# Kernel optimization log

Hardware: AMD Instinct MI355X
Metric: run time of the kernel (lower is better)

## Reference

```python
import jax, jax.numpy as jnp
import numpy as np

B, N, D, G = 32, 1024, 512, 32  # batch, set size, in_features, num_gaussians


def setup_inputs() -> dict:
    key = jax.random.key(0)
    k1, k2 = jax.random.split(key)
    minibatch = jax.random.normal(k1, (B, N, D), dtype=jnp.float32)
    # xavier_uniform for Linear(D -> G)
    limit = float(np.sqrt(6.0 / (D + G)))
    W_pi = jax.random.uniform(k2, (G, D), dtype=jnp.float32, minval=-limit, maxval=limit)
    b_pi = jnp.zeros((G,), dtype=jnp.float32)
    return {"minibatch": minibatch, "W_pi": W_pi, "b_pi": b_pi}


def reference(minibatch, W_pi, b_pi):
    d = minibatch.shape[-1]
    o = d // 2
    # mixture weights per (batch, sample): softmax over gaussian axis
    logits = jnp.einsum('bnd,gd->bng', minibatch, W_pi) + b_pi  # [B,N,G]
    pi = jax.nn.softmax(logits, axis=2)
    mu = minibatch[:, :, :o]        # [B,N,O]
    sigma = minibatch[:, :, -o:]    # [B,N,O]
    weights = jnp.mean(pi, axis=1)  # [B,G]
    denom = jnp.sum(pi, axis=1)     # [B,G]
    # weighted first moment -> locs (vectorized over all gaussians at once)
    m1 = jnp.einsum('bng,bno->bgo', pi, mu)                 # [B,G,O]
    locs = m1 / denom[:, :, None]                            # [B,G,O]
    # weighted E[mu^2 + sigma^2]; variance = E[mu^2+sigma^2] - locs^2
    # (identical math to sum(pi*((locs-mu)^2 + sigma^2))/sum(pi))
    m2 = jnp.einsum('bng,bno->bgo', pi, mu * mu + sigma * sigma)
    var = m2 / denom[:, :, None] - locs * locs
    scales = jnp.sqrt(jnp.maximum(var, 0.0))                 # [B,G,O]
    return weights, scales, locs
```

## Files before the change

kernel.cpp:

```cpp
#include <hip/hip_runtime.h>
#include <stdint.h>

#define B_ 32
#define N_ 1024
#define D_ 512
#define G_ 32

typedef __attribute__((ext_vector_type(8))) short short8;
typedef __attribute__((ext_vector_type(4))) float f32x4;
union U4S8 { uint4 u; short8 s; };

#define WS_M   524288
#define WS_DN  2621440

__device__ inline uint32_t pack_bf16x2(float a, float b) {
  uint32_t ua = __float_as_uint(a);
  uint32_t ub = __float_as_uint(b);
  ua += 0x7FFFu + ((ua >> 16) & 1u);
  ub += 0x7FFFu + ((ub >> 16) & 1u);
  return (ua >> 16) | (ub & 0xFFFF0000u);
}
__device__ inline uint16_t bf16r(float a) {
  uint32_t u = __float_as_uint(a);
  u += 0x7FFFu + ((u >> 16) & 1u);
  return (uint16_t)(u >> 16);
}

__global__ __launch_bounds__(256, 2) void mdn_k1(
    const float* __restrict__ x, const float* __restrict__ W,
    const float* __restrict__ bpi, float* ws)
{
  __shared__ uint32_t Wb[8192];
  __shared__ uint32_t SPT[1024];
  __shared__ float wpart[4][32];

  const int t = threadIdx.x;
  const int bid = blockIdx.x;
  const int b = bid >> 4;
  const int n0 = (bid & 15) * 64;
  const int w = t >> 6;
  const int lane = t & 63;

  #pragma unroll
  for (int i = 0; i < 8; ++i) {
    int s = t + i * 256;
    int g = s >> 6;
    int d0 = (s & 63) * 8;
    const float4* src = (const float4*)(W + g * D_ + d0);
    float4 f0 = src[0], f1 = src[1];
    int ks = d0 >> 5, ksub = (d0 >> 3) & 3;
    uint4 v;
    v.x = pack_bf16x2(f0.x, f0.y); v.y = pack_bf16x2(f0.z, f0.w);
    v.z = pack_bf16x2(f1.x, f1.y); v.w = pack_bf16x2(f1.z, f1.w);
    *(uint4*)(Wb + (size_t)(((ks * 4 + ksub) * 32 + g) * 4)) = v;
  }
  __syncthreads();

  const float* abase =
      x + ((size_t)(b * N_ + n0 + w * 16 + (lane & 15))) * D_ + (lane >> 4) * 8;

  f32x4 acc0 = {0.f, 0.f, 0.f, 0.f};
  f32x4 acc1 = {0.f, 0.f, 0.f, 0.f};

  float4 fa[16], fb[16];
  #pragma unroll
  for (int ks = 0; ks < 16; ++ks) {
    fa[ks] = *(const float4*)(abase + ks * 32);
    fb[ks] = *(const float4*)(abase + ks * 32 + 4);
  }
  #pragma unroll
  for (int ks = 0; ks < 16; ++ks) {
    U4S8 a;
    a.u.x = pack_bf16x2(fa[ks].x, fa[ks].y);
    a.u.y = pack_bf16x2(fa[ks].z, fa[ks].w);
    a.u.z = pack_bf16x2(fb[ks].x, fb[ks].y);
    a.u.w = pack_bf16x2(fb[ks].z, fb[ks].w);
    int idx = ((ks * 4 + (lane >> 4)) * 32 + (lane & 15)) * 4;
    U4S8 w0, w1;
    w0.u = *(uint4*)(Wb + idx);
    w1.u = *(uint4*)(Wb + idx + 64);
    acc0 = __builtin_amdgcn_mfma_f32_16x16x32_bf16(a.s, w0.s, acc0, 0, 0, 0);
    acc1 = __builtin_amdgcn_mfma_f32_16x16x32_bf16(a.s, w1.s, acc1, 0, 0, 0);
  }

  float bs0 = bpi[lane & 15], bs1 = bpi[16 + (lane & 15)];
  float pi0[4], pi1[4];
  float dsum0 = 0.f, dsum1 = 0.f;
  #pragma unroll
  for (int j = 0; j < 4; ++j) {
    float v0 = acc0[j] + bs0, v1 = acc1[j] + bs1;
    float m = fmaxf(v0, v1);
    m = fmaxf(m, __shfl_xor(m, 1));
    m = fmaxf(m, __shfl_xor(m, 2));
    m = fmaxf(m, __shfl_xor(m, 4));
    m = fmaxf(m, __shfl_xor(m, 8));
    float e0 = __expf(v0 - m), e1 = __expf(v1 - m);
    float s = e0 + e1;
    s += __shfl_xor(s, 1); s += __shfl_xor(s, 2);
    s += __shfl_xor(s, 4); s += __shfl_xor(s, 8);
    float inv = 1.0f / s;
    pi0[j] = e0 * inv; pi1[j] = e1 * inv;
    dsum0 += pi0[j];   dsum1 += pi1[j];
  }
  dsum0 += __shfl_xor(dsum0, 16); dsum0 += __shfl_xor(dsum0, 32);
  dsum1 += __shfl_xor(dsum1, 16); dsum1 += __shfl_xor(dsum1, 32);
  if (lane < 16) { wpart[w][lane] = dsum0; wpart[w][16 + lane] = dsum1; }

  {
    uint16_t* sp16 = (uint16_t*)SPT;
    int rl = w * 16 + (lane >> 4) * 4;
    #pragma unroll
    for (int j = 0; j < 4; ++j) {
      sp16[(lane & 15) * 64 + rl + j] = bf16r(pi0[j]);
      sp16[(16 + (lane & 15)) * 64 + rl + j] = bf16r(pi1[j]);
    }
  }
  __syncthreads();

  {
    int g = t >> 3, i = t & 7;
    uint4 v = *(uint4*)(SPT + g * 32 + i * 4);
    *(uint4*)((uint32_t*)ws + (size_t)(b * 32 + g) * 512 + (n0 >> 1) + i * 4) = v;
  }
  if (t < 32) {
    float s = wpart[0][t] + wpart[1][t] + wpart[2][t] + wpart[3][t];
    ws[WS_DN + bid * 32 + t] = s;
  }
}

__global__ __launch_bounds__(256, 2) void mdn_k2(
    const float* __restrict__ x, float* ws)
{
  const int t = threadIdx.x;
  const int bid = blockIdx.x;
  const int b = bid >> 4;
  const int kc = (bid >> 2) & 3;
  const int q = bid & 3;
  const int w = t >> 6;
  const int lane = t & 63;

  const uint32_t* piT = (const uint32_t*)ws;
  const uint32_t* pa0 =
      piT + (size_t)(b * 32 + (lane & 15)) * 512 + kc * 128 + (lane >> 4) * 4;
  const uint32_t* pa1 = pa0 + 16 * 512;

  const int ocol = q * 64 + w * 16 + (lane & 15);
  const float* xb =
      x + ((size_t)(b * N_) + kc * 256 + (lane >> 4) * 8) * D_ + ocol;

  f32x4 aM10 = {0.f,0.f,0.f,0.f}, aM11 = {0.f,0.f,0.f,0.f};
  f32x4 aM20 = {0.f,0.f,0.f,0.f}, aM21 = {0.f,0.f,0.f,0.f};

  #pragma unroll
  for (int ks = 0; ks < 8; ++ks) {
    U4S8 A0, A1;
    A0.u = *(const uint4*)(pa0 + ks * 16);
    A1.u = *(const uint4*)(pa1 + ks * 16);
    const float* xp = xb + (size_t)ks * 32 * D_;
    float mu[8], sg[8];
    #pragma unroll
    for (int i = 0; i < 8; ++i) {
      mu[i] = xp[i * D_];
      sg[i] = xp[i * D_ + 256];
    }
    U4S8 Bm, B2;
    Bm.u.x = pack_bf16x2(mu[0], mu[1]); Bm.u.y = pack_bf16x2(mu[2], mu[3]);
    Bm.u.z = pack_bf16x2(mu[4], mu[5]); Bm.u.w = pack_bf16x2(mu[6], mu[7]);
    float u0 = fmaf(mu[0], mu[0], sg[0] * sg[0]);
    float u1 = fmaf(mu[1], mu[1], sg[1] * sg[1]);
    float u2 = fmaf(mu[2], mu[2], sg[2] * sg[2]);
    float u3 = fmaf(mu[3], mu[3], sg[3] * sg[3]);
    float u4 = fmaf(mu[4], mu[4], sg[4] * sg[4]);
    float u5 = fmaf(mu[5], mu[5], sg[5] * sg[5]);
    float u6 = fmaf(mu[6], mu[6], sg[6] * sg[6]);
    float u7 = fmaf(mu[7], mu[7], sg[7] * sg[7]);
    B2.u.x = pack_bf16x2(u0, u1); B2.u.y = pack_bf16x2(u2, u3);
    B2.u.z = pack_bf16x2(u4, u5); B2.u.w = pack_bf16x2(u6, u7);
    aM10 = __builtin_amdgcn_mfma_f32_16x16x32_bf16(A0.s, Bm.s, aM10, 0, 0, 0);
    aM11 = __builtin_amdgcn_mfma_f32_16x16x32_bf16(A1.s, Bm.s, aM11, 0, 0, 0);
    aM20 = __builtin_amdgcn_mfma_f32_16x16x32_bf16(A0.s, B2.s, aM20, 0, 0, 0);
    aM21 = __builtin_amdgcn_mfma_f32_16x16x32_bf16(A1.s, B2.s, aM21, 0, 0, 0);
  }

  float* dst = ws + WS_M + (size_t)bid * 4096;
  const int cl = w * 16 + (lane & 15);
  #pragma unroll
  for (int j = 0; j < 4; ++j) {
    int g0 = (lane >> 4) * 4 + j;
    dst[g0 * 128 + cl] = aM10[j];
    dst[(16 + g0) * 128 + cl] = aM11[j];
    dst[g0 * 128 + 64 + cl] = aM20[j];
    dst[(16 + g0) * 128 + 64 + cl] = aM21[j];
  }
}

__global__ __launch_bounds__(256) void mdn_k3(
    const float* __restrict__ ws, float* __restrict__ out)
{
  __shared__ float dnm[G_];
  const int blk = blockIdx.x;
  const int b = blk >> 3, oc = blk & 7;
  const int t = threadIdx.x;
  if (t < G_) {
    float s = 0.f;
    #pragma unroll
    for (int c = 0; c < 16; ++c) s += ws[WS_DN + (b * 16 + c) * 32 + t];
    dnm[t] = s;
    if (oc == 0) out[b * G_ + t] = s * (1.0f / 1024.0f);
  }
  __syncthreads();
  const int g = t >> 3;
  const int o = oc * 32 + (t & 7) * 4;
  const int q = o >> 6;
  const int col = o & 63;
  float4 m1 = make_float4(0.f, 0.f, 0.f, 0.f);
  float4 m2 = make_float4(0.f, 0.f, 0.f, 0.f);
  #pragma unroll
  for (int kc = 0; kc < 4; ++kc) {
    const float* p = ws + WS_M + (size_t)((b * 16 + kc * 4 + q)) * 4096 + g * 128;
    float4 a = *(const float4*)(p + col);
    float4 c2 = *(const float4*)(p + 64 + col);
    m1.x += a.x; m1.y += a.y; m1.z += a.z; m1.w += a.w;
    m2.x += c2.x; m2.y += c2.y; m2.z += c2.z; m2.w += c2.w;
  }
  float inv = 1.0f / dnm[g];
  float4 lc = make_float4(m1.x * inv, m1.y * inv, m1.z * inv, m1.w * inv);
  float4 sc;
  sc.x = sqrtf(fmaxf(m2.x * inv - lc.x * lc.x, 0.f));
  sc.y = sqrtf(fmaxf(m2.y * inv - lc.y * lc.y, 0.f));
  sc.z = sqrtf(fmaxf(m2.z * inv - lc.z * lc.z, 0.f));
  sc.w = sqrtf(fmaxf(m2.w * inv - lc.w * lc.w, 0.f));
  float* scales = out + 1024;
  float* locs = out + 1024 + 262144;
  int oi = ((b * G_ + g) << 8) + o;
  *(float4*)(scales + oi) = sc;
  *(float4*)(locs + oi) = lc;
}

extern "C" void kernel_launch(void* const* d_in, const int* in_sizes, int n_in,
                              void* d_out, int out_size, void* d_ws, size_t ws_size,
                              hipStream_t stream)
{
  const float* x = (const float*)d_in[0];
  const float* W = (const float*)d_in[1];
  const float* bpi = (const float*)d_in[2];
  float* out = (float*)d_out;
  float* ws = (float*)d_ws;
  hipLaunchKernelGGL(mdn_k1, dim3(512), dim3(256), 0, stream, x, W, bpi, ws);
  hipLaunchKernelGGL(mdn_k2, dim3(512), dim3(256), 0, stream, x, ws);
  hipLaunchKernelGGL(mdn_k3, dim3(256), dim3(256), 0, stream, ws, out);
}
```

Baseline: 37.45 us.

## Precompute bf16 W once, shrink logits blocks, fuse moment reduction into k2

W is now converted to the bf16 MFMA fragment layout once in a small prologue kernel, so each logits block no longer repacks all of W into shared memory. The logits kernel moves to 128-thread blocks covering 32 rows with a two-phase load, which lowers register pressure. The moment kernel now runs 8 waves per block covering the full N range. It reduces partial moments through shared memory and computes locs, scales and weights itself, removing the third kernel and the global partial-sum round trip. The cost is an extra tiny launch, plus W fragments read from global or L2 instead of LDS.

Result: no change. 38.06 us (+1.6%).

```diff
diff --git a/kernel.cpp b/kernel.cpp
--- a/kernel.cpp
+++ b/kernel.cpp
@@ -10,8 +10,8 @@
 typedef __attribute__((ext_vector_type(4))) float f32x4;
 union U4S8 { uint4 u; short8 s; };
 
-#define WS_M   524288
-#define WS_DN  2621440
+#define WS_DN  524288
+#define WS_WF  557056
 
 __device__ inline uint32_t pack_bf16x2(float a, float b) {
   uint32_t ua = __float_as_uint(a);
@@ -26,61 +26,64 @@
   return (uint16_t)(u >> 16);
 }
 
-__global__ __launch_bounds__(256, 2) void mdn_k1(
-    const float* __restrict__ x, const float* __restrict__ W,
-    const float* __restrict__ bpi, float* ws)
-{
-  __shared__ uint32_t Wb[8192];
-  __shared__ uint32_t SPT[1024];
-  __shared__ float wpart[4][32];
+__global__ __launch_bounds__(256) void mdn_k0(
+    const float* __restrict__ W, float* ws)
+{
+  int s = blockIdx.x * 256 + threadIdx.x;
+  int g = s >> 6;
+  int d0 = (s & 63) * 8;
+  const float4* src = (const float4*)(W + g * D_ + d0);
+  float4 f0 = src[0], f1 = src[1];
+  int ks = d0 >> 5, ksub = (d0 >> 3) & 3;
+  uint4 v;
+  v.x = pack_bf16x2(f0.x, f0.y); v.y = pack_bf16x2(f0.z, f0.w);
+  v.z = pack_bf16x2(f1.x, f1.y); v.w = pack_bf16x2(f1.z, f1.w);
+  ((uint4*)(ws + WS_WF))[(ks * 4 + ksub) * 32 + g] = v;
+}
+
+__global__ __launch_bounds__(128, 2) void mdn_k1(
+    const float* __restrict__ x, const float* __restrict__ bpi, float* ws)
+{
+  __shared__ uint32_t SPT[512];
+  __shared__ float wpart[2][32];
 
   const int t = threadIdx.x;
   const int bid = blockIdx.x;
-  const int b = bid >> 4;
-  const int n0 = (bid & 15) * 64;
+  const int b = bid >> 5;
+  const int n0 = (bid & 31) * 32;
   const int w = t >> 6;
   const int lane = t & 63;
 
-  #pragma unroll
-  for (int i = 0; i < 8; ++i) {
-    int s = t + i * 256;
-    int g = s >> 6;
-    int d0 = (s & 63) * 8;
-    const float4* src = (const float4*)(W + g * D_ + d0);
-    float4 f0 = src[0], f1 = src[1];
-    int ks = d0 >> 5, ksub = (d0 >> 3) & 3;
-    uint4 v;
-    v.x = pack_bf16x2(f0.x, f0.y); v.y = pack_bf16x2(f0.z, f0.w);
-    v.z = pack_bf16x2(f1.x, f1.y); v.w = pack_bf16x2(f1.z, f1.w);
-    *(uint4*)(Wb + (size_t)(((ks * 4 + ksub) * 32 + g) * 4)) = v;
-  }
-  __syncthreads();
-
   const float* abase =
       x + ((size_t)(b * N_ + n0 + w * 16 + (lane & 15))) * D_ + (lane >> 4) * 8;
+  const uint4* wf4 = (const uint4*)(ws + WS_WF);
 
   f32x4 acc0 = {0.f, 0.f, 0.f, 0.f};
   f32x4 acc1 = {0.f, 0.f, 0.f, 0.f};
 
-  float4 fa[16], fb[16];
-  #pragma unroll
-  for (int ks = 0; ks < 16; ++ks) {
-    fa[ks] = *(const float4*)(abase + ks * 32);
-    fb[ks] = *(const float4*)(abase + ks * 32 + 4);
-  }
-  #pragma unroll
-  for (int ks = 0; ks < 16; ++ks) {
-    U4S8 a;
-    a.u.x = pack_bf16x2(fa[ks].x, fa[ks].y);
-    a.u.y = pack_bf16x2(fa[ks].z, fa[ks].w);
-    a.u.z = pack_bf16x2(fb[ks].x, fb[ks].y);
-    a.u.w = pack_bf16x2(fb[ks].z, fb[ks].w);
-    int idx = ((ks * 4 + (lane >> 4)) * 32 + (lane & 15)) * 4;
-    U4S8 w0, w1;
-    w0.u = *(uint4*)(Wb + idx);
-    w1.u = *(uint4*)(Wb + idx + 64);
-    acc0 = __builtin_amdgcn_mfma_f32_16x16x32_bf16(a.s, w0.s, acc0, 0, 0, 0);
-    acc1 = __builtin_amdgcn_mfma_f32_16x16x32_bf16(a.s, w1.s, acc1, 0, 0, 0);
+  #pragma unroll
+  for (int h = 0; h < 2; ++h) {
+    float4 fa[8], fb[8];
+    #pragma unroll
+    for (int k = 0; k < 8; ++k) {
+      const float* s = abase + (h * 8 + k) * 32;
+      fa[k] = *(const float4*)s; fb[k] = *(const float4*)(s + 4);
+    }
+    #pragma unroll
+    for (int k = 0; k < 8; ++k) {
+      int ks = h * 8 + k;
+      U4S8 a;
+      a.u.x = pack_bf16x2(fa[k].x, fa[k].y);
+      a.u.y = pack_bf16x2(fa[k].z, fa[k].w);
+      a.u.z = pack_bf16x2(fb[k].x, fb[k].y);
+      a.u.w = pack_bf16x2(fb[k].z, fb[k].w);
+      int wi = (ks * 4 + (lane >> 4)) * 32 + (lane & 15);
+      U4S8 w0, w1;
+      w0.u = wf4[wi];
+      w1.u = wf4[wi + 16];
+      acc0 = __builtin_amdgcn_mfma_f32_16x16x32_bf16(a.s, w0.s, acc0, 0, 0, 0);
+      acc1 = __builtin_amdgcn_mfma_f32_16x16x32_bf16(a.s, w1.s, acc1, 0, 0, 0);
+    }
   }
 
   float bs0 = bpi[lane & 15], bs1 = bpi[16 + (lane & 15)];
@@ -111,42 +114,53 @@
     int rl = w * 16 + (lane >> 4) * 4;
     #pragma unroll
     for (int j = 0; j < 4; ++j) {
-      sp16[(lane & 15) * 64 + rl + j] = bf16r(pi0[j]);
-      sp16[(16 + (lane & 15)) * 64 + rl + j] = bf16r(pi1[j]);
+      sp16[(lane & 15) * 32 + rl + j] = bf16r(pi0[j]);
+      sp16[(16 + (lane & 15)) * 32 + rl + j] = bf16r(pi1[j]);
     }
   }
   __syncthreads();
 
   {
-    int g = t >> 3, i = t & 7;
-    uint4 v = *(uint4*)(SPT + g * 32 + i * 4);
+    int g = t >> 2, i = t & 3;
+    uint4 v = *(uint4*)(SPT + g * 16 + i * 4);
     *(uint4*)((uint32_t*)ws + (size_t)(b * 32 + g) * 512 + (n0 >> 1) + i * 4) = v;
   }
   if (t < 32) {
-    float s = wpart[0][t] + wpart[1][t] + wpart[2][t] + wpart[3][t];
-    ws[WS_DN + bid * 32 + t] = s;
-  }
-}
-
-__global__ __launch_bounds__(256, 2) void mdn_k2(
-    const float* __restrict__ x, float* ws)
-{
+    ws[WS_DN + bid * 32 + t] = wpart[0][t] + wpart[1][t];
+  }
+}
+
+__global__ __launch_bounds__(512, 2) void mdn_k2(
+    const float* __restrict__ x, float* ws, float* __restrict__ out)
+{
+  __shared__ float dnm[G_];
+  __shared__ float RED[4][2][32][16][2];
+
   const int t = threadIdx.x;
   const int bid = blockIdx.x;
-  const int b = bid >> 4;
-  const int kc = (bid >> 2) & 3;
-  const int q = bid & 3;
+  const int b = bid >> 3;
+  const int q = bid & 7;
   const int w = t >> 6;
   const int lane = t & 63;
+  const int kh = w >> 1;
+  const int ot = w & 1;
+
+  if (t < G_) {
+    float s = 0.f;
+    #pragma unroll
+    for (int c = 0; c < 32; ++c) s += ws[WS_DN + (b * 32 + c) * 32 + t];
+    dnm[t] = s;
+    if (q == 0) out[b * G_ + t] = s * (1.0f / 1024.0f);
+  }
 
   const uint32_t* piT = (const uint32_t*)ws;
   const uint32_t* pa0 =
-      piT + (size_t)(b * 32 + (lane & 15)) * 512 + kc * 128 + (lane >> 4) * 4;
+      piT + (size_t)(b * 32 + (lane & 15)) * 512 + kh * 128 + (lane >> 4) * 4;
   const uint32_t* pa1 = pa0 + 16 * 512;
 
-  const int ocol = q * 64 + w * 16 + (lane & 15);
+  const int ocol = q * 32 + ot * 16 + (lane & 15);
   const float* xb =
-      x + ((size_t)(b * N_) + kc * 256 + (lane >> 4) * 8) * D_ + ocol;
+      x + ((size_t)(b * N_) + kh * 256 + (lane >> 4) * 8) * D_ + ocol;
 
   f32x4 aM10 = {0.f,0.f,0.f,0.f}, aM11 = {0.f,0.f,0.f,0.f};
   f32x4 aM20 = {0.f,0.f,0.f,0.f}, aM21 = {0.f,0.f,0.f,0.f};
@@ -182,59 +196,40 @@
     aM21 = __builtin_amdgcn_mfma_f32_16x16x32_bf16(A1.s, B2.s, aM21, 0, 0, 0);
   }
 
-  float* dst = ws + WS_M + (size_t)bid * 4096;
-  const int cl = w * 16 + (lane & 15);
   #pragma unroll
   for (int j = 0; j < 4; ++j) {
     int g0 = (lane >> 4) * 4 + j;
-    dst[g0 * 128 + cl] = aM10[j];
-    dst[(16 + g0) * 128 + cl] = aM11[j];
-    dst[g0 * 128 + 64 + cl] = aM20[j];
-    dst[(16 + g0) * 128 + 64 + cl] = aM21[j];
-  }
-}
-
-__global__ __launch_bounds__(256) void mdn_k3(
-    const float* __restrict__ ws, float* __restrict__ out)
-{
-  __shared__ float dnm[G_];
-  const int blk = blockIdx.x;
-  const int b = blk >> 3, oc = blk & 7;
-  const int t = threadIdx.x;
-  if (t < G_) {
-    float s = 0.f;
-    #pragma unroll
-    for (int c = 0; c < 16; ++c) s += ws[WS_DN + (b * 16 + c) * 32 + t];
-    dnm[t] = s;
-    if (oc == 0) out[b * G_ + t] = s * (1.0f / 1024.0f);
+    int cl = lane & 15;
+    RED[kh][ot][g0][cl][0] = aM10[j];
+    RED[kh][ot][g0][cl][1] = aM20[j];
+    RED[kh][ot][16 + g0][cl][0] = aM11[j];
+    RED[kh][ot][16 + g0][cl][1] = aM21[j];
   }
   __syncthreads();
-  const int g = t >> 3;
-  const int o = oc * 32 + (t & 7) * 4;
-  const int q = o >> 6;
-  const int col = o & 63;
-  float4 m1 = make_float4(0.f, 0.f, 0.f, 0.f);
-  float4 m2 = make_float4(0.f, 0.f, 0.f, 0.f);
-  #pragma unroll
-  for (int kc = 0; kc < 4; ++kc) {
-    const float* p = ws + WS_M + (size_t)((b * 16 + kc * 4 + q)) * 4096 + g * 128;
-    float4 a = *(const float4*)(p + col);
-    float4 c2 = *(const float4*)(p + 64 + col);
-    m1.x += a.x; m1.y += a.y; m1.z += a.z; m1.w += a.w;
-    m2.x += c2.x; m2.y += c2.y; m2.z += c2.z; m2.w += c2.w;
-  }
-  float inv = 1.0f / dnm[g];
-  float4 lc = make_float4(m1.x * inv, m1.y * inv, m1.z * inv, m1.w * inv);
-  float4 sc;
-  sc.x = sqrtf(fmaxf(m2.x * inv - lc.x * lc.x, 0.f));
-  sc.y = sqrtf(fmaxf(m2.y * inv - lc.y * lc.y, 0.f));
-  sc.z = sqrtf(fmaxf(m2.z * inv - lc.z * lc.z, 0.f));
-  sc.w = sqrtf(fmaxf(m2.w * inv - lc.w * lc.w, 0.f));
-  float* scales = out + 1024;
-  float* locs = out + 1024 + 262144;
-  int oi = ((b * G_ + g) << 8) + o;
-  *(float4*)(scales + oi) = sc;
-  *(float4*)(locs + oi) = lc;
+
+  if (t < 256) {
+    int g = t >> 3;
+    int col = (t & 7) * 4;
+    float inv = 1.0f / dnm[g];
+    float lc4[4], sc4[4];
+    #pragma unroll
+    for (int cc = 0; cc < 4; ++cc) {
+      int colc = col + cc;
+      int o2 = colc >> 4, cl = colc & 15;
+      float m1 = RED[0][o2][g][cl][0] + RED[1][o2][g][cl][0] +
+                 RED[2][o2][g][cl][0] + RED[3][o2][g][cl][0];
+      float m2 = RED[0][o2][g][cl][1] + RED[1][o2][g][cl][1] +
+                 RED[2][o2][g][cl][1] + RED[3][o2][g][cl][1];
+      float lc = m1 * inv;
+      lc4[cc] = lc;
+      sc4[cc] = sqrtf(fmaxf(m2 * inv - lc * lc, 0.f));
+    }
+    float* scales = out + 1024;
+    float* locs = out + 1024 + 262144;
+    int oi = ((b * G_ + g) << 8) + q * 32 + col;
+    *(float4*)(scales + oi) = make_float4(sc4[0], sc4[1], sc4[2], sc4[3]);
+    *(float4*)(locs + oi)   = make_float4(lc4[0], lc4[1], lc4[2], lc4[3]);
+  }
 }
 
 extern "C" void kernel_launch(void* const* d_in, const int* in_sizes, int n_in,
@@ -246,7 +241,7 @@
   const float* bpi = (const float*)d_in[2];
   float* out = (float*)d_out;
   float* ws = (float*)d_ws;
-  hipLaunchKernelGGL(mdn_k1, dim3(512), dim3(256), 0, stream, x, W, bpi, ws);
-  hipLaunchKernelGGL(mdn_k2, dim3(512), dim3(256), 0, stream, x, ws);
-  hipLaunchKernelGGL(mdn_k3, dim3(256), dim3(256), 0, stream, ws, out);
-}
+  hipLaunchKernelGGL(mdn_k0, dim3(8), dim3(256), 0, stream, W, ws);
+  hipLaunchKernelGGL(mdn_k1, dim3(1024), dim3(128), 0, stream, x, bpi, ws);
+  hipLaunchKernelGGL(mdn_k2, dim3(256), dim3(512), 0, stream, x, ws, out);
+}
```
